# Kernel tuning notes

Measured on AMD Instinct MI355X. Metric: run time of the kernel, lower is better.

Reference implementation:

```python
import jax, jax.numpy as jnp
import numpy as np

DIM = 256
QK_DIM = 256
SCALE = QK_DIM ** (-0.5)


def depthwise_conv3x3(x_img, w, b):
    # x_img: [B, C, H, W], w: [C, 1, 3, 3] (OIHW, groups=C), b: [C]
    out = jax.lax.conv_general_dilated(
        x_img, w, window_strides=(1, 1), padding='SAME',
        feature_group_count=x_img.shape[1],
        dimension_numbers=('NCHW', 'OIHW', 'NCHW'))
    return out + b[None, :, None, None]


def setup_inputs() -> dict:
    key = jax.random.key(0)
    ks = jax.random.split(key, 7)
    B, N, C = 4, 4096, DIM
    s = 0.02
    return {
        'x': jax.random.normal(ks[0], (B, N, C), jnp.float32),
        'W_qkv': jax.random.normal(ks[1], (C, 3 * C), jnp.float32) * s,
        'W_gate': jax.random.normal(ks[2], (C, C), jnp.float32) * s,
        'b_gate': jax.random.normal(ks[3], (C,), jnp.float32) * s,
        'W_proj': jax.random.normal(ks[4], (C, C), jnp.float32) * s,
        'pe_w': jax.random.normal(ks[5], (C, 1, 3, 3), jnp.float32) * s,
        'pe_b': jax.random.normal(ks[6], (C,), jnp.float32) * s,
    }


def reference(x, W_qkv, W_gate, b_gate, W_proj, pe_w, pe_b):
    B, N, C = x.shape
    ws = int(N ** 0.5)
    qkv = x @ W_qkv                               # [B, N, 3C]
    q, k, v = jnp.split(qkv, [QK_DIM, 2 * QK_DIM], axis=-1)
    z = jax.nn.gelu(x @ W_gate + b_gate, approximate=False)  # [B, N, C]
    # depthwise-conv positional encoding on q viewed as an image
    q_img = jnp.transpose(q, (0, 2, 1)).reshape(B, C, ws, ws)
    pe = depthwise_conv3x3(q_img, pe_w, pe_b).reshape(B, C, N)
    pe = jnp.transpose(pe, (0, 2, 1))             # [B, N, C]
    # single-head attention (heads arg unused in the original forward)
    attn = jax.nn.softmax(jnp.einsum('bnc,bmc->bnm', q, k) * SCALE, axis=-1)
    out = jnp.einsum('bnm,bmc->bnc', attn, v) + pe
    out = out * z
    return out @ W_proj
```

## Files before the change

### kernel.cpp

```cpp
#include <hip/hip_runtime.h>
#include <hip/hip_bf16.h>
#include <math.h>
#include <stdint.h>

typedef unsigned short u16;
typedef __attribute__((ext_vector_type(8))) short bf8;
typedef __attribute__((ext_vector_type(4))) float f4;

#define SC_LOG2E 0.09016844f

__device__ __forceinline__ float b2f(u16 u) {
    union { uint32_t i; float f; } v; v.i = ((uint32_t)u) << 16; return v.f;
}
__device__ __forceinline__ u16 f2b(float f) {
    union { float f; uint32_t i; } v; v.f = f;
    uint32_t r = (v.i + 0x7FFFu + ((v.i >> 16) & 1u)) >> 16;
    return (u16)r;
}
__device__ __forceinline__ uint32_t pk_bf16(float lo, float hi) {
    uint32_t r;
    asm("v_cvt_pk_bf16_f32 %0, %1, %2" : "=v"(r) : "v"(lo), "v"(hi));
    return r;
}

__global__ __launch_bounds__(256) void prep_weights(
        const float* __restrict__ Wqkv, const float* __restrict__ Wgate,
        const float* __restrict__ Wproj,
        u16* __restrict__ WT_all, u16* __restrict__ WTp) {
    int e = blockIdx.x * 256 + threadIdx.x;
    if (e < 262144) {
        int n = e >> 8, k = e & 255;
        WT_all[e] = f2b((n < 768) ? Wqkv[k * 768 + n] : Wgate[k * 256 + (n - 768)]);
    } else {
        int e2 = e - 262144;
        int n = e2 >> 8, k = e2 & 255;
        WTp[e2] = f2b(Wproj[k * 256 + n]);
    }
}

__global__ __launch_bounds__(256) void xcast(
        const float* __restrict__ x, u16* __restrict__ xb) {
    int i = (blockIdx.x * 256 + threadIdx.x) * 4;
    float4 f = *(const float4*)&x[i];
    uint2 o;
    o.x = pk_bf16(f.x, f.y);
    o.y = pk_bf16(f.z, f.w);
    *(uint2*)&xb[i] = o;
}

__global__ __launch_bounds__(512) void gemm_qkvz(
        const u16* __restrict__ xb, const u16* __restrict__ WT,
        const float* __restrict__ b_gate,
        u16* __restrict__ qo, u16* __restrict__ ko,
        u16* __restrict__ vT, u16* __restrict__ zo) {
    __shared__ u16 As[64 * 520];
    __shared__ u16 Bs[64 * 520];
    const int t = threadIdx.x;
    const int w = t >> 6, lane = t & 63, l15 = lane & 15, q4 = lane >> 4;
    const int m0 = blockIdx.x * 128;
    const int by = blockIdx.y;
    const int n0 = by * 128;

    const int lo = lane >> 5;
    const int lcn = ((lane & 31) - 4 * lo) & 31;

    auto stage128 = [&](const u16* src, u16* dst) {
#pragma unroll
        for (int rr = 0; rr < 8; rr++) {
            int pp = rr * 8 + w;
            const u16* g = src + (size_t)(pp * 2 + lo) * 256 + lcn * 8;
            __builtin_amdgcn_global_load_lds(
                (const __attribute__((address_space(1))) unsigned int*)g,
                (__attribute__((address_space(3))) unsigned int*)&dst[pp * 520],
                16, 0, 0);
        }
    };
    auto kaddr = [&](const u16* base, int row, int cn) -> const u16* {
        int o = row & 1;
        return base + (row >> 1) * 520 + o * 256 + (((cn + 4 * o) & 31) << 3);
    };

    stage128(&xb[(size_t)m0 * 256], As);
    stage128(&WT[(size_t)n0 * 256], Bs);
    __syncthreads();

    const int mtb = (w & 3) * 32;
    const int ntb = (w >> 2) * 64;
    const bool vTout = (by >> 1) == 2;

    f4 acc[2][4];
#pragma unroll
    for (int i = 0; i < 2; i++)
#pragma unroll
        for (int j = 0; j < 4; j++) acc[i][j] = (f4){0.f, 0.f, 0.f, 0.f};

#pragma unroll
    for (int c = 0; c < 8; c++) {
        bf8 af0 = *(const bf8*)kaddr(As, mtb + l15, c * 4 + q4);
        bf8 af1 = *(const bf8*)kaddr(As, mtb + 16 + l15, c * 4 + q4);
        if (vTout) {
#pragma unroll
            for (int j = 0; j < 4; j++) {
                bf8 bfj = *(const bf8*)kaddr(Bs, ntb + j * 16 + l15, c * 4 + q4);
                acc[0][j] = __builtin_amdgcn_mfma_f32_16x16x32_bf16(af0, bfj, acc[0][j], 0, 0, 0);
                acc[1][j] = __builtin_amdgcn_mfma_f32_16x16x32_bf16(af1, bfj, acc[1][j], 0, 0, 0);
            }
        } else {
#pragma unroll
            for (int j = 0; j < 4; j++) {
                bf8 bfj = *(const bf8*)kaddr(Bs, ntb + j * 16 + l15, c * 4 + q4);
                acc[0][j] = __builtin_amdgcn_mfma_f32_16x16x32_bf16(bfj, af0, acc[0][j], 0, 0, 0);
                acc[1][j] = __builtin_amdgcn_mfma_f32_16x16x32_bf16(bfj, af1, acc[1][j], 0, 0, 0);
            }
        }
    }

    const int kind = by >> 1;
    const int colbase = (by & 1) * 128;

    if (kind == 2) {
        int bb = m0 >> 12;
        int nnb = (m0 & 4095) + mtb + q4 * 4;
#pragma unroll
        for (int i = 0; i < 2; i++) {
            int nn = nnb + i * 16;
#pragma unroll
            for (int j = 0; j < 4; j++) {
                int vc = colbase + ntb + j * 16 + l15;
                uint2 pk;
                pk.x = pk_bf16(acc[i][j][0], acc[i][j][1]);
                pk.y = pk_bf16(acc[i][j][2], acc[i][j][3]);
                *(uint2*)&vT[(size_t)(bb * 256 + vc) * 4096 + nn] = pk;
            }
        }
    } else if (kind == 3) {
#pragma unroll
        for (int i = 0; i < 2; i++) {
            size_t mrow = (size_t)(m0 + mtb + i * 16 + l15) * 256 + colbase;
#pragma unroll
            for (int j = 0; j < 4; j++) {
                int col = ntb + j * 16 + q4 * 4;
                float4 bg4 = *(const float4*)&b_gate[colbase + col];
                float v0 = acc[i][j][0] + bg4.x;
                float v1 = acc[i][j][1] + bg4.y;
                float v2 = acc[i][j][2] + bg4.z;
                float v3 = acc[i][j][3] + bg4.w;
                v0 = 0.5f * v0 * (1.0f + erff(v0 * 0.70710678118654752f));
                v1 = 0.5f * v1 * (1.0f + erff(v1 * 0.70710678118654752f));
                v2 = 0.5f * v2 * (1.0f + erff(v2 * 0.70710678118654752f));
                v3 = 0.5f * v3 * (1.0f + erff(v3 * 0.70710678118654752f));
                uint2 o;
                o.x = pk_bf16(v0, v1);
                o.y = pk_bf16(v2, v3);
                *(uint2*)&zo[mrow + col] = o;
            }
        }
    } else {
        u16* dst = (kind == 0) ? qo : ko;
#pragma unroll
        for (int i = 0; i < 2; i++) {
            size_t mrow = (size_t)(m0 + mtb + i * 16 + l15) * 256 + colbase;
#pragma unroll
            for (int j = 0; j < 4; j++) {
                int col = ntb + j * 16 + q4 * 4;
                uint2 o;
                o.x = pk_bf16(acc[i][j][0], acc[i][j][1]);
                o.y = pk_bf16(acc[i][j][2], acc[i][j][3]);
                *(uint2*)&dst[mrow + col] = o;
            }
        }
    }
}

__global__ __launch_bounds__(256) void conv_pe(
        const u16* __restrict__ q, const float* __restrict__ pw,
        const float* __restrict__ pb, u16* __restrict__ pe) {
    const int bid = blockIdx.x;
    const int b = bid >> 8, h = (bid >> 2) & 63, wsg = bid & 3;
    const int c = threadIdx.x;
    float wgt[9];
#pragma unroll
    for (int i = 0; i < 9; i++) wgt[i] = pw[c * 9 + i];
    const float bias = pb[c];
    const u16* qb = q + b * (4096 * 256);
    u16* peb = pe + b * (4096 * 256);
    const bool vTop = h > 0, vBot = h < 63;
    const u16* rT = qb + (h - 1) * 64 * 256 + c;
    const u16* rM = qb + h * 64 * 256 + c;
    const u16* rB = qb + (h + 1) * 64 * 256 + c;
    const int w0 = wsg * 16;

    float t0, t1, t2, m0v, m1, m2, b0, b1, b2v;
    if (w0 > 0) {
        int o = (w0 - 1) * 256;
        t0 = vTop ? b2f(rT[o]) : 0.f;
        m0v = b2f(rM[o]);
        b0 = vBot ? b2f(rB[o]) : 0.f;
    } else { t0 = 0.f; m0v = 0.f; b0 = 0.f; }
    {
        int o = w0 * 256;
        t1 = vTop ? b2f(rT[o]) : 0.f;
        m1 = b2f(rM[o]);
        b1 = vBot ? b2f(rB[o]) : 0.f;
    }
#pragma unroll
    for (int w2 = 0; w2 < 16; ++w2) {
        int wn = w0 + w2 + 1;
        if (wn < 64) {
            int o = wn * 256;
            t2 = vTop ? b2f(rT[o]) : 0.f;
            m2 = b2f(rM[o]);
            b2v = vBot ? b2f(rB[o]) : 0.f;
        } else { t2 = 0.f; m2 = 0.f; b2v = 0.f; }
        float acc = bias
            + wgt[0] * t0 + wgt[1] * t1 + wgt[2] * t2
            + wgt[3] * m0v + wgt[4] * m1 + wgt[5] * m2
            + wgt[6] * b0 + wgt[7] * b1 + wgt[8] * b2v;
        peb[(h * 64 + w0 + w2) * 256 + c] = f2b(acc);
        t0 = t1; t1 = t2; m0v = m1; m1 = m2; b0 = b1; b1 = b2v;
    }
}

__global__ __launch_bounds__(512) void attn(
        const u16* __restrict__ q, const u16* __restrict__ k,
        const u16* __restrict__ vT, const u16* __restrict__ pe,
        const u16* __restrict__ z, u16* __restrict__ u) {
    __shared__ u16 Kst[32 * 520];
    __shared__ u16 Vs2[2][256 * 64];
    __shared__ u16 Ps[64 * 72];
    __shared__ float l_part[8][64];

    const int t = threadIdx.x;
    const int w = t >> 6, lane = t & 63, l15 = lane & 15, q4 = lane >> 4;
    const int kg = w >> 1, qh = w & 1;
    const int xcd = blockIdx.x & 7;
    const int b = xcd >> 1;
    const int qt = (blockIdx.x >> 3) * 2 + (xcd & 1);
    const int m0 = b * 4096 + qt * 64;

    const u16* kb = k + (size_t)b * 4096 * 256;
    const u16* vbase = vT + (size_t)b * 256 * 4096;

    const int lo = lane >> 5;
    const int lcn = ((lane & 31) - 4 * lo) & 31;

    auto stage64 = [&](const u16* src) {
#pragma unroll
        for (int rr = 0; rr < 4; rr++) {
            int pp = rr * 8 + w;
            const u16* g = src + (size_t)(pp * 2 + lo) * 256 + lcn * 8;
            u16* l = &Kst[pp * 520];
            __builtin_amdgcn_global_load_lds(
                (const __attribute__((address_space(1))) unsigned int*)g,
                (__attribute__((address_space(3))) unsigned int*)l, 16, 0, 0);
        }
    };
    const int vrl = lane >> 3, vsl = lane & 7;
    auto stageV = [&](const u16* src, u16* dst) {
#pragma unroll
        for (int j = 0; j < 4; j++) {
            int op = j * 8 + w;
            int r = op * 8 + vrl;
            int cn = (vsl - r) & 7;
            const u16* g = src + (size_t)r * 4096 + cn * 8;
            u16* l = dst + op * 512;
            __builtin_amdgcn_global_load_lds(
                (const __attribute__((address_space(1))) unsigned int*)g,
                (__attribute__((address_space(3))) unsigned int*)l, 16, 0, 0);
        }
    };
    auto kaddr = [&](int row, int cn) -> const u16* {
        int o = row & 1;
        return &Kst[(row >> 1) * 520 + o * 256 + (((cn + 4 * o) & 31) << 3)];
    };

    stage64(q + (size_t)m0 * 256);
    __syncthreads();
    bf8 qf[2][8];
#pragma unroll
    for (int qtt = 0; qtt < 2; qtt++)
#pragma unroll
        for (int c = 0; c < 8; c++)
            qf[qtt][c] = *(const bf8*)kaddr(qh * 32 + qtt * 16 + l15, c * 4 + q4);
    __syncthreads();

    stage64(kb);
    stageV(vbase, Vs2[0]);

    f4 O[2][4];
#pragma unroll
    for (int vg = 0; vg < 2; vg++)
#pragma unroll
        for (int qg = 0; qg < 4; qg++) O[vg][qg] = (f4){0.f, 0.f, 0.f, 0.f};
    float lrow[2] = {0.f, 0.f};

    auto body = [&](int kt, const u16* Vcur, u16* Vnxt) {
        __syncthreads();

        f4 St[2];
        St[0] = (f4){0.f, 0.f, 0.f, 0.f};
        St[1] = (f4){0.f, 0.f, 0.f, 0.f};
        __builtin_amdgcn_s_setprio(1);
#pragma unroll
        for (int c = 0; c < 8; c++) {
            bf8 kf = *(const bf8*)kaddr(kg * 16 + l15, c * 4 + q4);
            St[0] = __builtin_amdgcn_mfma_f32_16x16x32_bf16(kf, qf[0][c], St[0], 0, 0, 0);
            St[1] = __builtin_amdgcn_mfma_f32_16x16x32_bf16(kf, qf[1][c], St[1], 0, 0, 0);
        }
        __builtin_amdgcn_s_setprio(0);

#pragma unroll
        for (int qtt = 0; qtt < 2; qtt++) {
            float e0 = exp2f(fminf(fmaxf(St[qtt][0] * SC_LOG2E, -30.f), 30.f));
            float e1 = exp2f(fminf(fmaxf(St[qtt][1] * SC_LOG2E, -30.f), 30.f));
            float e2 = exp2f(fminf(fmaxf(St[qtt][2] * SC_LOG2E, -30.f), 30.f));
            float e3 = exp2f(fminf(fmaxf(St[qtt][3] * SC_LOG2E, -30.f), 30.f));
            uint2 pk;
            pk.x = pk_bf16(e0, e1);
            pk.y = pk_bf16(e2, e3);
            int qrow = qh * 32 + qtt * 16 + l15;
            *(uint2*)&Ps[qrow * 72 + kg * 16 + q4 * 4] = pk;
            float s = (e0 + e1) + (e2 + e3);
            s += __shfl_xor(s, 16);
            s += __shfl_xor(s, 32);
            lrow[qtt] += s;
        }
        __syncthreads();

        if (kt < 63) {
            stage64(kb + (size_t)(kt + 1) * 16384);
            stageV(vbase + (size_t)(kt + 1) * 64, Vnxt);
        }

        bf8 pf[4][2], vfr[2][2];
#pragma unroll
        for (int qg = 0; qg < 4; qg++)
#pragma unroll
            for (int kh = 0; kh < 2; kh++)
                pf[qg][kh] = *(bf8*)&Ps[(qg * 16 + l15) * 72 + kh * 32 + q4 * 8];
#pragma unroll
        for (int vg = 0; vg < 2; vg++)
#pragma unroll
            for (int kh = 0; kh < 2; kh++) {
                int R = w * 32 + vg * 16 + l15;
                int slot = ((kh * 4 + q4) + R) & 7;
                vfr[vg][kh] = *(const bf8*)&Vcur[R * 64 + slot * 8];
            }
        __builtin_amdgcn_s_setprio(1);
#pragma unroll
        for (int vg = 0; vg < 2; vg++)
#pragma unroll
            for (int qg = 0; qg < 4; qg++) {
                O[vg][qg] = __builtin_amdgcn_mfma_f32_16x16x32_bf16(
                    vfr[vg][0], pf[qg][0], O[vg][qg], 0, 0, 0);
                O[vg][qg] = __builtin_amdgcn_mfma_f32_16x16x32_bf16(
                    vfr[vg][1], pf[qg][1], O[vg][qg], 0, 0, 0);
            }
        __builtin_amdgcn_s_setprio(0);
    };

    for (int kt2 = 0; kt2 < 64; kt2 += 2) {
        body(kt2,     Vs2[0], Vs2[1]);
        body(kt2 + 1, Vs2[1], Vs2[0]);
    }

    if (q4 == 0) {
        l_part[w][qh * 32 + l15] = lrow[0];
        l_part[w][qh * 32 + 16 + l15] = lrow[1];
    }
    __syncthreads();

#pragma unroll
    for (int qg = 0; qg < 4; qg++) {
        int qrow = qg * 16 + l15;
        int qhq = qg >> 1;
        float lt = l_part[qhq][qrow] + l_part[2 + qhq][qrow]
                 + l_part[4 + qhq][qrow] + l_part[6 + qhq][qrow];
        float linv = 1.0f / lt;
        size_t mrow = (size_t)(m0 + qrow) * 256;
#pragma unroll
        for (int vg = 0; vg < 2; vg++) {
            int vcb = w * 32 + vg * 16 + q4 * 4;
            ushort4 pe4 = *(const ushort4*)&pe[mrow + vcb];
            ushort4 z4  = *(const ushort4*)&z[mrow + vcb];
            float r0 = (O[vg][qg][0] * linv + b2f(pe4.x)) * b2f(z4.x);
            float r1 = (O[vg][qg][1] * linv + b2f(pe4.y)) * b2f(z4.y);
            float r2 = (O[vg][qg][2] * linv + b2f(pe4.z)) * b2f(z4.z);
            float r3 = (O[vg][qg][3] * linv + b2f(pe4.w)) * b2f(z4.w);
            uint2 o4;
            o4.x = pk_bf16(r0, r1);
            o4.y = pk_bf16(r2, r3);
            *(uint2*)&u[mrow + vcb] = o4;
        }
    }
}

__global__ __launch_bounds__(512) void gemm_proj(
        const u16* __restrict__ u, const u16* __restrict__ WTp,
        float* __restrict__ out) {
    __shared__ u16 As[64 * 520];
    __shared__ u16 Bs[64 * 520];
    const int t = threadIdx.x;
    const int w = t >> 6, lane = t & 63, l15 = lane & 15, q4 = lane >> 4;
    const int m0 = blockIdx.x * 128;
    const int n0 = blockIdx.y * 128;

    const int lo = lane >> 5;
    const int lcn = ((lane & 31) - 4 * lo) & 31;

    auto stage128 = [&](const u16* src, u16* dst) {
#pragma unroll
        for (int rr = 0; rr < 8; rr++) {
            int pp = rr * 8 + w;
            const u16* g = src + (size_t)(pp * 2 + lo) * 256 + lcn * 8;
            __builtin_amdgcn_global_load_lds(
                (const __attribute__((address_space(1))) unsigned int*)g,
                (__attribute__((address_space(3))) unsigned int*)&dst[pp * 520],
                16, 0, 0);
        }
    };
    auto kaddr = [&](const u16* base, int row, int cn) -> const u16* {
        int o = row & 1;
        return base + (row >> 1) * 520 + o * 256 + (((cn + 4 * o) & 31) << 3);
    };

    stage128(&u[(size_t)m0 * 256], As);
    stage128(&WTp[(size_t)n0 * 256], Bs);
    __syncthreads();

    const int mtb = (w & 3) * 32;
    const int ntb = (w >> 2) * 64;

    f4 acc[2][4];
#pragma unroll
    for (int i = 0; i < 2; i++)
#pragma unroll
        for (int j = 0; j < 4; j++) acc[i][j] = (f4){0.f, 0.f, 0.f, 0.f};

#pragma unroll
    for (int c = 0; c < 8; c++) {
        bf8 af0 = *(const bf8*)kaddr(As, mtb + l15, c * 4 + q4);
        bf8 af1 = *(const bf8*)kaddr(As, mtb + 16 + l15, c * 4 + q4);
#pragma unroll
        for (int j = 0; j < 4; j++) {
            bf8 bfj = *(const bf8*)kaddr(Bs, ntb + j * 16 + l15, c * 4 + q4);
            acc[0][j] = __builtin_amdgcn_mfma_f32_16x16x32_bf16(bfj, af0, acc[0][j], 0, 0, 0);
            acc[1][j] = __builtin_amdgcn_mfma_f32_16x16x32_bf16(bfj, af1, acc[1][j], 0, 0, 0);
        }
    }

#pragma unroll
    for (int i = 0; i < 2; i++) {
        float* orow = &out[(size_t)(m0 + mtb + i * 16 + l15) * 256 + n0];
#pragma unroll
        for (int j = 0; j < 4; j++) {
            *(f4*)&orow[ntb + j * 16 + q4 * 4] = acc[i][j];
        }
    }
}

extern "C" void kernel_launch(void* const* d_in, const int* in_sizes, int n_in,
                              void* d_out, int out_size, void* d_ws, size_t ws_size,
                              hipStream_t stream) {
    (void)in_sizes; (void)n_in; (void)out_size; (void)ws_size;
    const float* x      = (const float*)d_in[0];
    const float* Wqkv   = (const float*)d_in[1];
    const float* Wgate  = (const float*)d_in[2];
    const float* bgate  = (const float*)d_in[3];
    const float* Wproj  = (const float*)d_in[4];
    const float* pw     = (const float*)d_in[5];
    const float* pb     = (const float*)d_in[6];
    float* out = (float*)d_out;

    char* ws = (char*)d_ws;
    u16* WT_all = (u16*)(ws);
    u16* WTp    = (u16*)(ws + 524288);
    u16* q      = (u16*)(ws + 655360);
    u16* k      = (u16*)(ws + 9043968);
    u16* vT     = (u16*)(ws + 17432576);
    u16* z      = (u16*)(ws + 25821184);
    u16* pe     = (u16*)(ws + 34209792);
    u16* u      = (u16*)(ws + 42598400);

    u16* xb = u;

    prep_weights<<<1280, 256, 0, stream>>>(Wqkv, Wgate, Wproj, WT_all, WTp);
    xcast<<<4096, 256, 0, stream>>>(x, xb);
    gemm_qkvz<<<dim3(128, 8), 512, 0, stream>>>(xb, WT_all, bgate, q, k, vT, z);
    conv_pe<<<1024, 256, 0, stream>>>(q, pw, pb, pe);
    attn<<<256, 512, 0, stream>>>(q, k, vT, pe, z, u);
    gemm_proj<<<dim3(128, 2), 512, 0, stream>>>(u, WTp, out);
}
```

Baseline: 232.2 us.

## Fuse output projection into attention epilogue and merge weight prep with x cast

```diff
diff --git a/kernel.cpp b/kernel.cpp
--- a/kernel.cpp
+++ b/kernel.cpp
@@ -23,29 +23,30 @@
     return r;
 }
 
-__global__ __launch_bounds__(256) void prep_weights(
+__global__ __launch_bounds__(256) void prep_all(
         const float* __restrict__ Wqkv, const float* __restrict__ Wgate,
-        const float* __restrict__ Wproj,
-        u16* __restrict__ WT_all, u16* __restrict__ WTp) {
-    int e = blockIdx.x * 256 + threadIdx.x;
-    if (e < 262144) {
-        int n = e >> 8, k = e & 255;
-        WT_all[e] = f2b((n < 768) ? Wqkv[k * 768 + n] : Wgate[k * 256 + (n - 768)]);
+        const float* __restrict__ Wproj, const float* __restrict__ x,
+        u16* __restrict__ WT_all, u16* __restrict__ WTp,
+        u16* __restrict__ xb) {
+    int bid = blockIdx.x;
+    if (bid < 1280) {
+        int e = bid * 256 + threadIdx.x;
+        if (e < 262144) {
+            int n = e >> 8, k = e & 255;
+            WT_all[e] = f2b((n < 768) ? Wqkv[k * 768 + n] : Wgate[k * 256 + (n - 768)]);
+        } else {
+            int e2 = e - 262144;
+            int n = e2 >> 8, k = e2 & 255;
+            WTp[e2] = f2b(Wproj[k * 256 + n]);
+        }
     } else {
-        int e2 = e - 262144;
-        int n = e2 >> 8, k = e2 & 255;
-        WTp[e2] = f2b(Wproj[k * 256 + n]);
-    }
-}
-
-__global__ __launch_bounds__(256) void xcast(
-        const float* __restrict__ x, u16* __restrict__ xb) {
-    int i = (blockIdx.x * 256 + threadIdx.x) * 4;
-    float4 f = *(const float4*)&x[i];
-    uint2 o;
-    o.x = pk_bf16(f.x, f.y);
-    o.y = pk_bf16(f.z, f.w);
-    *(uint2*)&xb[i] = o;
+        int i = ((bid - 1280) * 256 + threadIdx.x) * 4;
+        float4 f = *(const float4*)&x[i];
+        uint2 o;
+        o.x = pk_bf16(f.x, f.y);
+        o.y = pk_bf16(f.z, f.w);
+        *(uint2*)&xb[i] = o;
+    }
 }
 
 __global__ __launch_bounds__(512) void gemm_qkvz(
@@ -224,7 +225,8 @@
 __global__ __launch_bounds__(512) void attn(
         const u16* __restrict__ q, const u16* __restrict__ k,
         const u16* __restrict__ vT, const u16* __restrict__ pe,
-        const u16* __restrict__ z, u16* __restrict__ u) {
+        const u16* __restrict__ z, const u16* __restrict__ WTp,
+        float* __restrict__ out) {
     __shared__ u16 Kst[32 * 520];
     __shared__ u16 Vs2[2][256 * 64];
     __shared__ u16 Ps[64 * 72];
@@ -370,6 +372,7 @@
     }
     __syncthreads();
 
+    u16* Us = Kst;
 #pragma unroll
     for (int qg = 0; qg < 4; qg++) {
         int qrow = qg * 16 + l15;
@@ -390,72 +393,54 @@
             uint2 o4;
             o4.x = pk_bf16(r0, r1);
             o4.y = pk_bf16(r2, r3);
-            *(uint2*)&u[mrow + vcb] = o4;
-        }
-    }
-}
-
-__global__ __launch_bounds__(512) void gemm_proj(
-        const u16* __restrict__ u, const u16* __restrict__ WTp,
-        float* __restrict__ out) {
-    __shared__ u16 As[64 * 520];
-    __shared__ u16 Bs[64 * 520];
-    const int t = threadIdx.x;
-    const int w = t >> 6, lane = t & 63, l15 = lane & 15, q4 = lane >> 4;
-    const int m0 = blockIdx.x * 128;
-    const int n0 = blockIdx.y * 128;
-
-    const int lo = lane >> 5;
-    const int lcn = ((lane & 31) - 4 * lo) & 31;
-
-    auto stage128 = [&](const u16* src, u16* dst) {
-#pragma unroll
-        for (int rr = 0; rr < 8; rr++) {
-            int pp = rr * 8 + w;
-            const u16* g = src + (size_t)(pp * 2 + lo) * 256 + lcn * 8;
+            int cn = vcb >> 3;
+            int slot = (cn + qrow) & 31;
+            *(uint2*)&Us[qrow * 256 + slot * 8 + (vcb & 7)] = o4;
+        }
+    }
+
+    auto stageW = [&](const u16* src, u16* dst) {
+#pragma unroll
+        for (int j = 0; j < 4; j++) {
+            int op = j * 8 + w;
+            int r = op * 2 + lo;
+            int cn = ((lane & 31) - r) & 31;
+            const u16* g = src + (size_t)r * 256 + cn * 8;
             __builtin_amdgcn_global_load_lds(
                 (const __attribute__((address_space(1))) unsigned int*)g,
-                (__attribute__((address_space(3))) unsigned int*)&dst[pp * 520],
+                (__attribute__((address_space(3))) unsigned int*)&dst[op * 512],
                 16, 0, 0);
         }
     };
-    auto kaddr = [&](const u16* base, int row, int cn) -> const u16* {
-        int o = row & 1;
-        return base + (row >> 1) * 520 + o * 256 + (((cn + 4 * o) & 31) << 3);
-    };
-
-    stage128(&u[(size_t)m0 * 256], As);
-    stage128(&WTp[(size_t)n0 * 256], Bs);
+
+    stageW(WTp, (u16*)Vs2[0]);
     __syncthreads();
 
-    const int mtb = (w & 3) * 32;
-    const int ntb = (w >> 2) * 64;
-
-    f4 acc[2][4];
-#pragma unroll
-    for (int i = 0; i < 2; i++)
-#pragma unroll
-        for (int j = 0; j < 4; j++) acc[i][j] = (f4){0.f, 0.f, 0.f, 0.f};
-
-#pragma unroll
-    for (int c = 0; c < 8; c++) {
-        bf8 af0 = *(const bf8*)kaddr(As, mtb + l15, c * 4 + q4);
-        bf8 af1 = *(const bf8*)kaddr(As, mtb + 16 + l15, c * 4 + q4);
-#pragma unroll
-        for (int j = 0; j < 4; j++) {
-            bf8 bfj = *(const bf8*)kaddr(Bs, ntb + j * 16 + l15, c * 4 + q4);
-            acc[0][j] = __builtin_amdgcn_mfma_f32_16x16x32_bf16(bfj, af0, acc[0][j], 0, 0, 0);
-            acc[1][j] = __builtin_amdgcn_mfma_f32_16x16x32_bf16(bfj, af1, acc[1][j], 0, 0, 0);
-        }
-    }
-
-#pragma unroll
-    for (int i = 0; i < 2; i++) {
-        float* orow = &out[(size_t)(m0 + mtb + i * 16 + l15) * 256 + n0];
-#pragma unroll
-        for (int j = 0; j < 4; j++) {
-            *(f4*)&orow[ntb + j * 16 + q4 * 4] = acc[i][j];
-        }
+    const int mtl = (w & 3) * 16;
+    const int ntl = (w >> 2) * 32;
+#pragma unroll
+    for (int nq = 0; nq < 4; nq++) {
+        if (nq < 3) stageW(WTp + (size_t)(nq + 1) * 64 * 256, (u16*)Vs2[(nq + 1) & 1]);
+        const u16* Wl = (const u16*)Vs2[nq & 1];
+        f4 a0 = (f4){0.f, 0.f, 0.f, 0.f};
+        f4 a1 = (f4){0.f, 0.f, 0.f, 0.f};
+        const int mrowL = mtl + l15;
+        const int ln0 = ntl + l15, ln1 = ntl + 16 + l15;
+        __builtin_amdgcn_s_setprio(1);
+#pragma unroll
+        for (int c = 0; c < 8; c++) {
+            int cc = c * 4 + q4;
+            bf8 af = *(const bf8*)&Us[mrowL * 256 + (((cc + mrowL) & 31) << 3)];
+            bf8 b0 = *(const bf8*)&Wl[ln0 * 256 + (((cc + ln0) & 31) << 3)];
+            bf8 b1 = *(const bf8*)&Wl[ln1 * 256 + (((cc + ln1) & 31) << 3)];
+            a0 = __builtin_amdgcn_mfma_f32_16x16x32_bf16(b0, af, a0, 0, 0, 0);
+            a1 = __builtin_amdgcn_mfma_f32_16x16x32_bf16(b1, af, a1, 0, 0, 0);
+        }
+        __builtin_amdgcn_s_setprio(0);
+        float* ob = &out[(size_t)(m0 + mrowL) * 256 + nq * 64 + ntl];
+        *(f4*)&ob[q4 * 4] = a0;
+        *(f4*)&ob[16 + q4 * 4] = a1;
+        __syncthreads();
     }
 }
 
@@ -480,14 +465,10 @@
     u16* vT     = (u16*)(ws + 17432576);
     u16* z      = (u16*)(ws + 25821184);
     u16* pe     = (u16*)(ws + 34209792);
-    u16* u      = (u16*)(ws + 42598400);
-
-    u16* xb = u;
-
-    prep_weights<<<1280, 256, 0, stream>>>(Wqkv, Wgate, Wproj, WT_all, WTp);
-    xcast<<<4096, 256, 0, stream>>>(x, xb);
+    u16* xb     = (u16*)(ws + 42598400);
+
+    prep_all<<<5376, 256, 0, stream>>>(Wqkv, Wgate, Wproj, x, WT_all, WTp, xb);
     gemm_qkvz<<<dim3(128, 8), 512, 0, stream>>>(xb, WT_all, bgate, q, k, vT, z);
     conv_pe<<<1024, 256, 0, stream>>>(q, pw, pb, pe);
-    attn<<<256, 512, 0, stream>>>(q, k, vT, pe, z, u);
-    gemm_proj<<<dim3(128, 2), 512, 0, stream>>>(u, WTp, out);
-}
+    attn<<<256, 512, 0, stream>>>(q, k, vT, pe, z, WTp, out);
+}
```

Result: no change. 227.9 us (-1.8%).
